# Optimization experiments

Measured on AMD Instinct MI355X. Metric: run time of the kernel, lower is better.

## Reference

```python
import jax, jax.numpy as jnp
import numpy as np

L, B, D = 2048, 8, 1024
EPS = 1e-5  # torch LayerNorm default


def setup_inputs() -> dict:
    key = jax.random.key(0)
    k1, k2 = jax.random.split(key)
    x = jax.random.normal(k1, (L, B, D), dtype=jnp.float32)
    c = jnp.zeros((B, D), dtype=jnp.float32)
    W_ufr = 0.02 * jax.random.normal(k2, (3 * D, D), dtype=jnp.float32)
    ln_gamma = jnp.ones((D,), dtype=jnp.float32)
    ln_beta = jnp.zeros((D,), dtype=jnp.float32)
    return {"x": x, "c": c, "W_ufr": W_ufr, "ln_gamma": ln_gamma, "ln_beta": ln_beta}


def reference(x, c, W_ufr, ln_gamma, ln_beta):
    # LayerNorm over last dim
    mean = jnp.mean(x, axis=-1, keepdims=True)
    var = jnp.mean(jnp.square(x - mean), axis=-1, keepdims=True)
    x_norm = (x - mean) * jax.lax.rsqrt(var + EPS) * ln_gamma + ln_beta

    # Linear (no bias): [L,B,D] @ [D,3D]
    ufr = jnp.einsum('lbd,ed->lbe', x_norm, W_ufr)
    u, f, r = jnp.split(ufr, 3, axis=-1)
    f_gate = jax.nn.sigmoid(f)
    r_gate = jax.nn.sigmoid(r)

    # Sequential recurrence: c_t = f_t * c_{t-1} + (1 - f_t) * u_t
    def step(c_prev, fu):
        f_t, u_t = fu
        c_t = f_t * c_prev + (1.0 - f_t) * u_t
        return c_t, c_t

    last_c, c_stack = jax.lax.scan(step, c, (f_gate, u))

    hs = r_gate * jnp.tanh(c_stack) + (1.0 - r_gate) * x_norm
    return x + hs, last_c
```

## Files before the change

### kernel.cpp

```cpp
#include <hip/hip_runtime.h>
#include <hip/hip_bf16.h>
#include <stdint.h>

#define L_DIM 2048
#define B_DIM 8
#define D_DIM 1024
#define M_DIM (L_DIM * B_DIM)
#define N_DIM (3 * D_DIM)
#define K_DIM D_DIM
#define CH    (B_DIM * D_DIM)
#define EPSLN 1e-5f
#define NC 128
#define CL (L_DIM / NC)

typedef __attribute__((ext_vector_type(8))) short short8;
typedef __attribute__((ext_vector_type(4))) float floatx4;

static __device__ __forceinline__ float bf16_lo(unsigned int p) {
    union { unsigned int u; float f; } v; v.u = p << 16; return v.f;
}
static __device__ __forceinline__ float bf16_hi(unsigned int p) {
    union { unsigned int u; float f; } v; v.u = p & 0xffff0000u; return v.f;
}
static __device__ __forceinline__ unsigned short f32_to_bf16(float f) {
    union { float f; unsigned int u; } v;
    v.f = f;
    unsigned int u = v.u;
    u += 0x7fffu + ((u >> 16) & 1u);
    return (unsigned short)(u >> 16);
}
static __device__ __forceinline__ float sigmoidf_fast(float v) {
    return 1.0f / (1.0f + __expf(-v));
}
static __device__ __forceinline__ float tanhf_fast(float c) {
    return 1.0f - 2.0f / (1.0f + __expf(2.0f * c));
}

static __device__ __forceinline__ void async16(const void* g, void* l) {
    __builtin_amdgcn_global_load_lds(
        (const __attribute__((address_space(1))) unsigned int*)g,
        (__attribute__((address_space(3))) unsigned int*)l,
        16, 0, 0);
}

__global__ __launch_bounds__(256) void ln_kernel(const float* __restrict__ x,
                                                 const float* __restrict__ gamma,
                                                 const float* __restrict__ beta,
                                                 unsigned short* __restrict__ xn,
                                                 float* __restrict__ meanOut,
                                                 float* __restrict__ rstdOut) {
    const int row = blockIdx.x;
    const int tid = threadIdx.x;
    const float4* xr = (const float4*)(x + (size_t)row * D_DIM);
    float4 v = xr[tid];
    float s  = v.x + v.y + v.z + v.w;
    float s2 = v.x * v.x + v.y * v.y + v.z * v.z + v.w * v.w;
    #pragma unroll
    for (int o = 32; o > 0; o >>= 1) {
        s  += __shfl_xor(s, o, 64);
        s2 += __shfl_xor(s2, o, 64);
    }
    __shared__ float red[8];
    const int wid = tid >> 6;
    if ((tid & 63) == 0) { red[wid] = s; red[4 + wid] = s2; }
    __syncthreads();
    s  = red[0] + red[1] + red[2] + red[3];
    s2 = red[4] + red[5] + red[6] + red[7];
    const float mean = s * (1.0f / D_DIM);
    const float var  = s2 * (1.0f / D_DIM) - mean * mean;
    const float rstd = rsqrtf(var + EPSLN);
    if (tid == 0) { meanOut[row] = mean; rstdOut[row] = rstd; }
    const int col = tid * 4;
    const float4 g = *(const float4*)(gamma + col);
    const float4 b = *(const float4*)(beta + col);
    unsigned short o0 = f32_to_bf16((v.x - mean) * rstd * g.x + b.x);
    unsigned short o1 = f32_to_bf16((v.y - mean) * rstd * g.y + b.y);
    unsigned short o2 = f32_to_bf16((v.z - mean) * rstd * g.z + b.z);
    unsigned short o3 = f32_to_bf16((v.w - mean) * rstd * g.w + b.w);
    uint2 packed;
    packed.x = (unsigned int)o0 | ((unsigned int)o1 << 16);
    packed.y = (unsigned int)o2 | ((unsigned int)o3 << 16);
    *(uint2*)(xn + (size_t)row * D_DIM + col) = packed;
}

__global__ __launch_bounds__(256) void wconv_kernel(const float* __restrict__ W,
                                                    unsigned short* __restrict__ Wb) {
    const size_t i = ((size_t)blockIdx.x * 256 + threadIdx.x) * 4;
    float4 v = *(const float4*)(W + i);
    uint2 packed;
    packed.x = (unsigned int)f32_to_bf16(v.x) | ((unsigned int)f32_to_bf16(v.y) << 16);
    packed.y = (unsigned int)f32_to_bf16(v.z) | ((unsigned int)f32_to_bf16(v.w) << 16);
    *(uint2*)(Wb + i) = packed;
}

__global__ __launch_bounds__(256) void gemm_kernel(const unsigned short* __restrict__ A,
                                                   const unsigned short* __restrict__ W,
                                                   unsigned short* __restrict__ u,
                                                   unsigned short* __restrict__ f,
                                                   unsigned short* __restrict__ r) {
    __shared__ __align__(16) unsigned short ldsA[128 * 64];
    __shared__ __align__(16) unsigned short ldsB[128 * 64];
    const int tid  = threadIdx.x;
    const int m0   = blockIdx.y * 128;
    const int n0   = blockIdx.x * 128;
    const int wave = tid >> 6;
    const int lane = tid & 63;
    const int quad = lane >> 4;
    const int l16  = lane & 15;
    const int wm   = (wave >> 1) * 64;
    const int wn   = (wave & 1) * 64;

    floatx4 acc[4][4] = {};

    const int rowS   = tid >> 3;
    const int chunkS = (tid & 7) ^ (rowS & 7);
    const int kgS    = chunkS * 8;

    const unsigned short* gA = A + (size_t)(m0 + rowS) * K_DIM + kgS;
    const unsigned short* gB = W + (size_t)(n0 + rowS) * K_DIM + kgS;

    const int posX = l16 & 7;

    for (int k0 = 0; k0 < K_DIM; k0 += 64) {
        #pragma unroll
        for (int p = 0; p < 4; p++) {
            async16(gA + k0 + (size_t)(p * 32) * K_DIM, &ldsA[(size_t)(p * 256 + tid) * 8]);
            async16(gB + k0 + (size_t)(p * 32) * K_DIM, &ldsB[(size_t)(p * 256 + tid) * 8]);
        }
        __syncthreads();

        #pragma unroll
        for (int s = 0; s < 2; s++) {
            const int pos = (quad + 4 * s) ^ posX;
            short8 a[4], b[4];
            #pragma unroll
            for (int i = 0; i < 4; i++) {
                a[i] = *(const short8*)&ldsA[(wm + i * 16 + l16) * 64 + pos * 8];
                b[i] = *(const short8*)&ldsB[(wn + i * 16 + l16) * 64 + pos * 8];
            }
            #pragma unroll
            for (int i = 0; i < 4; i++)
                #pragma unroll
                for (int j = 0; j < 4; j++)
                    acc[i][j] = __builtin_amdgcn_mfma_f32_16x16x32_bf16(a[i], b[j], acc[i][j], 0, 0, 0);
        }
        __syncthreads();
    }

    const int region = n0 >> 10;
    const int nn0 = (n0 & 1023) + wn;
    unsigned short* dst = (region == 0) ? u : ((region == 1) ? f : r);
    const bool sig = (region != 0);
    #pragma unroll
    for (int i = 0; i < 4; i++) {
        #pragma unroll
        for (int j = 0; j < 4; j++) {
            #pragma unroll
            for (int t = 0; t < 4; t++) {
                const int gm = m0 + wm + i * 16 + quad * 4 + t;
                const int nn = nn0 + j * 16 + l16;
                float v = acc[i][j][t];
                if (sig) v = sigmoidf_fast(v);
                dst[(size_t)gm * D_DIM + nn] = f32_to_bf16(v);
            }
        }
    }
}

__global__ __launch_bounds__(256) void scan_reduce(const unsigned short* __restrict__ f,
                                                   const unsigned short* __restrict__ u,
                                                   float* __restrict__ Ac,
                                                   float* __restrict__ bc) {
    const int ch2   = (blockIdx.x * 256 + threadIdx.x) * 2;
    const int chunk = blockIdx.y;
    const size_t base = (size_t)chunk * CL * CH + ch2;
    float A0 = 1.0f, b0 = 0.0f, A1 = 1.0f, b1 = 0.0f;
    #pragma unroll
    for (int i = 0; i < CL; i++) {
        const size_t idx = base + (size_t)i * CH;
        const unsigned int fp = *(const unsigned int*)(f + idx);
        const unsigned int up = *(const unsigned int*)(u + idx);
        const float f0 = bf16_lo(fp), f1 = bf16_hi(fp);
        const float u0 = bf16_lo(up), u1 = bf16_hi(up);
        b0 = f0 * (b0 - u0) + u0;
        b1 = f1 * (b1 - u1) + u1;
        A0 *= f0;
        A1 *= f1;
    }
    *(float2*)(Ac + chunk * CH + ch2) = make_float2(A0, A1);
    *(float2*)(bc + chunk * CH + ch2) = make_float2(b0, b1);
}

__global__ __launch_bounds__(256) void scan_spine(const float* __restrict__ Ac,
                                                  const float* __restrict__ bc,
                                                  const float* __restrict__ c0,
                                                  float* __restrict__ cst) {
    const int ch = blockIdx.x * 256 + threadIdx.x;
    float c = c0[ch];
    #pragma unroll 16
    for (int j = 0; j < NC; j++) {
        cst[j * CH + ch] = c;
        c = Ac[j * CH + ch] * c + bc[j * CH + ch];
    }
}

__global__ __launch_bounds__(256) void scan_apply(const unsigned short* __restrict__ f,
                                                  const unsigned short* __restrict__ u,
                                                  const unsigned short* __restrict__ r,
                                                  const float* __restrict__ x,
                                                  const float* __restrict__ meanIn,
                                                  const float* __restrict__ rstdIn,
                                                  const float* __restrict__ gamma,
                                                  const float* __restrict__ beta,
                                                  const float* __restrict__ cst,
                                                  float* __restrict__ out,
                                                  float* __restrict__ lastc) {
    const int ch2   = (blockIdx.x * 256 + threadIdx.x) * 2;
    const int chunk = blockIdx.y;
    const int bidx  = ch2 >> 10;
    const int d     = ch2 & 1023;
    const float2 g  = *(const float2*)(gamma + d);
    const float2 be = *(const float2*)(beta + d);
    const size_t base = (size_t)chunk * CL * CH + ch2;
    float2 cc = *(const float2*)(cst + chunk * CH + ch2);
    float c0v = cc.x, c1v = cc.y;
    #pragma unroll 4
    for (int i = 0; i < CL; i++) {
        const int rowLB = (chunk * CL + i) * B_DIM + bidx;
        const float mu = meanIn[rowLB];
        const float rs = rstdIn[rowLB];
        const size_t idx = base + (size_t)i * CH;
        const unsigned int fp = *(const unsigned int*)(f + idx);
        const unsigned int up = *(const unsigned int*)(u + idx);
        const unsigned int rp = *(const unsigned int*)(r + idx);
        const float2 xv = *(const float2*)(x + idx);
        const float f0 = bf16_lo(fp), f1 = bf16_hi(fp);
        const float u0 = bf16_lo(up), u1 = bf16_hi(up);
        c0v = f0 * (c0v - u0) + u0;
        c1v = f1 * (c1v - u1) + u1;
        const float r0 = bf16_lo(rp), r1 = bf16_hi(rp);
        const float n0 = (xv.x - mu) * rs * g.x + be.x;
        const float n1 = (xv.y - mu) * rs * g.y + be.y;
        float2 o;
        o.x = xv.x + r0 * tanhf_fast(c0v) + (1.0f - r0) * n0;
        o.y = xv.y + r1 * tanhf_fast(c1v) + (1.0f - r1) * n1;
        *(float2*)(out + idx) = o;
    }
    if (chunk == NC - 1) *(float2*)(lastc + ch2) = make_float2(c0v, c1v);
}

extern "C" void kernel_launch(void* const* d_in, const int* in_sizes, int n_in,
                              void* d_out, int out_size, void* d_ws, size_t ws_size,
                              hipStream_t stream) {
    const float* x     = (const float*)d_in[0];
    const float* c0    = (const float*)d_in[1];
    const float* W     = (const float*)d_in[2];
    const float* gamma = (const float*)d_in[3];
    const float* beta  = (const float*)d_in[4];

    float* out   = (float*)d_out;
    float* lastc = out + (size_t)M_DIM * D_DIM;

    char* ws = (char*)d_ws;
    unsigned short* xn = (unsigned short*)ws;  ws += (size_t)M_DIM * K_DIM * 2;
    unsigned short* Wb = (unsigned short*)ws;  ws += (size_t)N_DIM * K_DIM * 2;
    unsigned short* u  = (unsigned short*)ws;  ws += (size_t)M_DIM * D_DIM * 2;
    unsigned short* f  = (unsigned short*)ws;  ws += (size_t)M_DIM * D_DIM * 2;
    unsigned short* r  = (unsigned short*)ws;  ws += (size_t)M_DIM * D_DIM * 2;
    float* meanBuf = (float*)ws;               ws += (size_t)M_DIM * 4;
    float* rstdBuf = (float*)ws;               ws += (size_t)M_DIM * 4;
    float* Ac  = (float*)ws;                   ws += (size_t)NC * CH * 4;
    float* bc  = (float*)ws;                   ws += (size_t)NC * CH * 4;
    float* cst = (float*)ws;                   ws += (size_t)NC * CH * 4;

    ln_kernel<<<M_DIM, 256, 0, stream>>>(x, gamma, beta, xn, meanBuf, rstdBuf);
    wconv_kernel<<<(N_DIM * K_DIM) / 1024, 256, 0, stream>>>(W, Wb);
    gemm_kernel<<<dim3(N_DIM / 128, M_DIM / 128), 256, 0, stream>>>(xn, Wb, u, f, r);
    scan_reduce<<<dim3(CH / 512, NC), 256, 0, stream>>>(f, u, Ac, bc);
    scan_spine<<<CH / 256, 256, 0, stream>>>(Ac, bc, c0, cst);
    scan_apply<<<dim3(CH / 512, NC), 256, 0, stream>>>(f, u, r, x, meanBuf, rstdBuf,
                                                       gamma, beta, cst, out, lastc);
}
```

Baseline: 316.0 us.

## Rewrite GEMM as 256x256 double-buffered pipelined tile with workgroup swizzle

Replaces the 128x128 single-buffered bf16 MFMA GEMM with a 256x256 tile, 512 threads and double-buffered LDS. Global-to-LDS async loads for the next K step are interleaved across four compute phases with explicit barriers, waitcnt and setprio. Block indices are swizzled to improve L2 reuse. This aims to hide memory latency and raise arithmetic intensity, at the cost of 128KB of LDS, higher register pressure and fragile hand-written synchronisation.

```diff
diff --git a/kernel.cpp b/kernel.cpp
--- a/kernel.cpp
+++ b/kernel.cpp
@@ -12,6 +12,14 @@
 #define EPSLN 1e-5f
 #define NC 128
 #define CL (L_DIM / NC)
+
+#define BM 256
+#define BN 256
+#define BK 64
+#define NT (K_DIM / BK)
+#define GX (N_DIM / BN)
+#define GY (M_DIM / BM)
+#define NWG (GX * GY)
 
 typedef __attribute__((ext_vector_type(8))) short short8;
 typedef __attribute__((ext_vector_type(4))) float floatx4;
@@ -93,75 +101,151 @@
     *(uint2*)(Wb + i) = packed;
 }
 
-__global__ __launch_bounds__(256) void gemm_kernel(const unsigned short* __restrict__ A,
-                                                   const unsigned short* __restrict__ W,
-                                                   unsigned short* __restrict__ u,
-                                                   unsigned short* __restrict__ f,
-                                                   unsigned short* __restrict__ r) {
-    __shared__ __align__(16) unsigned short ldsA[128 * 64];
-    __shared__ __align__(16) unsigned short ldsB[128 * 64];
+__global__ __launch_bounds__(512, 2) void gemm_kernel(const unsigned short* __restrict__ A,
+                                                      const unsigned short* __restrict__ W,
+                                                      unsigned short* __restrict__ u,
+                                                      unsigned short* __restrict__ f,
+                                                      unsigned short* __restrict__ r) {
+    __shared__ __align__(16) unsigned short ldsA[2][BM * BK];
+    __shared__ __align__(16) unsigned short ldsB[2][BM * BK];
+
     const int tid  = threadIdx.x;
-    const int m0   = blockIdx.y * 128;
-    const int n0   = blockIdx.x * 128;
     const int wave = tid >> 6;
     const int lane = tid & 63;
     const int quad = lane >> 4;
     const int l16  = lane & 15;
-    const int wm   = (wave >> 1) * 64;
-    const int wn   = (wave & 1) * 64;
-
-    floatx4 acc[4][4] = {};
-
-    const int rowS   = tid >> 3;
-    const int chunkS = (tid & 7) ^ (rowS & 7);
-    const int kgS    = chunkS * 8;
-
-    const unsigned short* gA = A + (size_t)(m0 + rowS) * K_DIM + kgS;
-    const unsigned short* gB = W + (size_t)(n0 + rowS) * K_DIM + kgS;
-
-    const int posX = l16 & 7;
-
-    for (int k0 = 0; k0 < K_DIM; k0 += 64) {
-        #pragma unroll
-        for (int p = 0; p < 4; p++) {
-            async16(gA + k0 + (size_t)(p * 32) * K_DIM, &ldsA[(size_t)(p * 256 + tid) * 8]);
-            async16(gB + k0 + (size_t)(p * 32) * K_DIM, &ldsB[(size_t)(p * 256 + tid) * 8]);
-        }
-        __syncthreads();
-
-        #pragma unroll
-        for (int s = 0; s < 2; s++) {
-            const int pos = (quad + 4 * s) ^ posX;
-            short8 a[4], b[4];
-            #pragma unroll
-            for (int i = 0; i < 4; i++) {
-                a[i] = *(const short8*)&ldsA[(wm + i * 16 + l16) * 64 + pos * 8];
-                b[i] = *(const short8*)&ldsB[(wn + i * 16 + l16) * 64 + pos * 8];
-            }
-            #pragma unroll
-            for (int i = 0; i < 4; i++)
-                #pragma unroll
-                for (int j = 0; j < 4; j++)
-                    acc[i][j] = __builtin_amdgcn_mfma_f32_16x16x32_bf16(a[i], b[j], acc[i][j], 0, 0, 0);
-        }
-        __syncthreads();
-    }
+    const int wr   = wave >> 2;
+    const int wc   = wave & 3;
+
+    const int orig = blockIdx.y * GX + blockIdx.x;
+    const int swz  = (orig & 7) * (NWG / 8) + (orig >> 3);
+    const int tx   = swz % GX;
+    const int ty   = swz / GX;
+    const int m0   = ty * BM;
+    const int n0   = tx * BN;
+
+    const int rS = tid >> 3;
+    const int kS = ((tid & 7) ^ (rS & 7)) * 8;
+    const unsigned short* gA = A + (size_t)(m0 + rS) * K_DIM + kS;
+    const unsigned short* gB = W + (size_t)(n0 + rS) * K_DIM + kS;
+
+    const int px     = l16 & 7;
+    const int p0_8   = (quad ^ px) * 8;
+    const int p1_8   = ((quad + 4) ^ px) * 8;
+    const int l16_64 = l16 * 64;
+    const int wr4096 = wr * 4096;
+    const int wc2048 = wc * 2048;
+
+    floatx4 acc[2][2][4][2] = {};
+    short8 a[4][2];
+    short8 b[2][2][2];
+
+#define STAGE_A(B_, KT_, H_) do { \
+    async16(gA + (size_t)((H_) * 128) * K_DIM + (size_t)(KT_) * 64, \
+            &ldsA[B_][(H_) * 8192 + (size_t)tid * 8]); \
+    async16(gA + (size_t)((H_) * 128 + 64) * K_DIM + (size_t)(KT_) * 64, \
+            &ldsA[B_][(H_) * 8192 + 4096 + (size_t)tid * 8]); \
+} while (0)
+
+#define STAGE_B(B_, KT_, H_) do { \
+    async16(gB + (size_t)((H_) * 128) * K_DIM + (size_t)(KT_) * 64, \
+            &ldsB[B_][(H_) * 8192 + (size_t)tid * 8]); \
+    async16(gB + (size_t)((H_) * 128 + 64) * K_DIM + (size_t)(KT_) * 64, \
+            &ldsB[B_][(H_) * 8192 + 4096 + (size_t)tid * 8]); \
+} while (0)
+
+#define RD_A(MH_) do { \
+    const unsigned short* pa_ = &ldsA[buf][(MH_) * 8192 + wr4096 + l16_64]; \
+    _Pragma("unroll") \
+    for (int i_ = 0; i_ < 4; i_++) { \
+        a[i_][0] = *(const short8*)(pa_ + i_ * 1024 + p0_8); \
+        a[i_][1] = *(const short8*)(pa_ + i_ * 1024 + p1_8); \
+    } \
+} while (0)
+
+#define RD_B(NH_) do { \
+    const unsigned short* pb_ = &ldsB[buf][(NH_) * 8192 + wc2048 + l16_64]; \
+    _Pragma("unroll") \
+    for (int j_ = 0; j_ < 2; j_++) { \
+        b[NH_][j_][0] = *(const short8*)(pb_ + j_ * 1024 + p0_8); \
+        b[NH_][j_][1] = *(const short8*)(pb_ + j_ * 1024 + p1_8); \
+    } \
+} while (0)
+
+#define PHASE(RDSTMT, STAGESTMT, MH_, NH_, VM_) do { \
+    RDSTMT; \
+    STAGESTMT; \
+    __builtin_amdgcn_s_barrier(); \
+    asm volatile("s_waitcnt lgkmcnt(0)" ::: "memory"); \
+    __builtin_amdgcn_sched_barrier(0); \
+    __builtin_amdgcn_s_setprio(1); \
+    _Pragma("unroll") \
+    for (int i_ = 0; i_ < 4; i_++) { \
+        _Pragma("unroll") \
+        for (int j_ = 0; j_ < 2; j_++) { \
+            acc[MH_][NH_][i_][j_] = __builtin_amdgcn_mfma_f32_16x16x32_bf16( \
+                a[i_][0], b[NH_][j_][0], acc[MH_][NH_][i_][j_], 0, 0, 0); \
+            acc[MH_][NH_][i_][j_] = __builtin_amdgcn_mfma_f32_16x16x32_bf16( \
+                a[i_][1], b[NH_][j_][1], acc[MH_][NH_][i_][j_], 0, 0, 0); \
+        } \
+    } \
+    __builtin_amdgcn_s_setprio(0); \
+    __builtin_amdgcn_sched_barrier(0); \
+    asm volatile("s_waitcnt vmcnt(" VM_ ")" ::: "memory"); \
+    __builtin_amdgcn_s_barrier(); \
+    asm volatile("" ::: "memory"); \
+} while (0)
+
+    STAGE_A(0, 0, 0); STAGE_A(0, 0, 1);
+    STAGE_B(0, 0, 0); STAGE_B(0, 0, 1);
+    asm volatile("s_waitcnt vmcnt(0)" ::: "memory");
+    __builtin_amdgcn_s_barrier();
+    asm volatile("" ::: "memory");
+
+    for (int kt = 0; kt < NT - 1; ++kt) {
+        const int buf  = kt & 1;
+        const int nbuf = buf ^ 1;
+        PHASE({ RD_A(0); RD_B(0); }, STAGE_A(nbuf, kt + 1, 0), 0, 0, "4");
+        PHASE(RD_B(1),               STAGE_B(nbuf, kt + 1, 0), 0, 1, "4");
+        PHASE(RD_A(1),               STAGE_B(nbuf, kt + 1, 1), 1, 1, "4");
+        PHASE((void)0,               STAGE_A(nbuf, kt + 1, 1), 1, 0, "4");
+    }
+
+    {
+        const int buf = (NT - 1) & 1;
+        PHASE({ RD_A(0); RD_B(0); }, (void)0, 0, 0, "2");
+        PHASE(RD_B(1),               (void)0, 0, 1, "0");
+        PHASE(RD_A(1),               (void)0, 1, 1, "0");
+        PHASE((void)0,               (void)0, 1, 0, "0");
+    }
+
+#undef PHASE
+#undef RD_A
+#undef RD_B
+#undef STAGE_A
+#undef STAGE_B
 
     const int region = n0 >> 10;
-    const int nn0 = (n0 & 1023) + wn;
+    const int nnb = n0 & 1023;
     unsigned short* dst = (region == 0) ? u : ((region == 1) ? f : r);
     const bool sig = (region != 0);
     #pragma unroll
-    for (int i = 0; i < 4; i++) {
+    for (int mh = 0; mh < 2; mh++) {
         #pragma unroll
-        for (int j = 0; j < 4; j++) {
+        for (int nh = 0; nh < 2; nh++) {
             #pragma unroll
-            for (int t = 0; t < 4; t++) {
-                const int gm = m0 + wm + i * 16 + quad * 4 + t;
-                const int nn = nn0 + j * 16 + l16;
-                float v = acc[i][j][t];
-                if (sig) v = sigmoidf_fast(v);
-                dst[(size_t)gm * D_DIM + nn] = f32_to_bf16(v);
+            for (int i = 0; i < 4; i++) {
+                #pragma unroll
+                for (int j = 0; j < 2; j++) {
+                    #pragma unroll
+                    for (int t = 0; t < 4; t++) {
+                        const int gm = m0 + mh * 128 + wr * 64 + i * 16 + quad * 4 + t;
+                        const int nn = nnb + nh * 128 + wc * 32 + j * 16 + l16;
+                        float v = acc[mh][nh][i][j][t];
+                        if (sig) v = sigmoidf_fast(v);
+                        dst[(size_t)gm * D_DIM + nn] = f32_to_bf16(v);
+                    }
+                }
             }
         }
     }
@@ -275,7 +359,7 @@
 
     ln_kernel<<<M_DIM, 256, 0, stream>>>(x, gamma, beta, xn, meanBuf, rstdBuf);
     wconv_kernel<<<(N_DIM * K_DIM) / 1024, 256, 0, stream>>>(W, Wb);
-    gemm_kernel<<<dim3(N_DIM / 128, M_DIM / 128), 256, 0, stream>>>(xn, Wb, u, f, r);
+    gemm_kernel<<<dim3(GX, GY), 512, 0, stream>>>(xn, Wb, u, f, r);
     scan_reduce<<<dim3(CH / 512, NC), 256, 0, stream>>>(f, u, Ac, bc);
     scan_spine<<<CH / 256, 256, 0, stream>>>(Ac, bc, c0, cst);
     scan_apply<<<dim3(CH / 512, NC), 256, 0, stream>>>(f, u, r, x, meanBuf, rstdBuf,
```

Measured after the change: 299.7 us. -5.2%, faster.
